# Kernel optimization log

Hardware: AMD Instinct MI355X
Metric: run time of the kernel (lower is better)

The kernel has to match this reference:

```python
import jax, jax.numpy as jnp
import numpy as np

D_MODEL = 1024
N_HEADS = 16
D_HEAD = D_MODEL // N_HEADS
BLOCK = 128
B, T = 2, 2048


def setup_inputs() -> dict:
    key = jax.random.key(0)
    ks = jax.random.split(key, 5)
    x = jax.random.normal(ks[0], (B, T, D_MODEL), dtype=jnp.float32)
    def init_w(k):
        # nn.Linear default init scale ~ 1/sqrt(fan_in)
        return jax.random.normal(k, (D_MODEL, D_MODEL), dtype=jnp.float32) / np.sqrt(D_MODEL).astype(np.float32)
    return {
        "x": x,
        "Wq": init_w(ks[1]),
        "Wk": init_w(ks[2]),
        "Wv": init_w(ks[3]),
        "Wo": init_w(ks[4]),
    }


def _flash_attention(Q, K, V, block_size, scale):
    """Online-softmax tiled attention over kv blocks (causal). Q,K,V: (B,H,T,d)."""
    Bb, H, Tt, d = Q.shape
    n_blocks = Tt // block_size
    # (n_blocks, B, H, block, d) so scan streams kv tiles
    Kb = K.reshape(Bb, H, n_blocks, block_size, d).transpose(2, 0, 1, 3, 4)
    Vb = V.reshape(Bb, H, n_blocks, block_size, d).transpose(2, 0, 1, 3, 4)
    starts = jnp.arange(n_blocks) * block_size
    q_pos = jnp.arange(Tt)

    def step(carry, xs):
        m, l, acc = carry
        kb, vb, st = xs
        # scores: (B,H,T,block)
        scores = scale * jnp.einsum('bhtd,bhsd->bhts', Q, kb)
        kv_pos = st + jnp.arange(block_size)
        future = kv_pos[None, :] > q_pos[:, None]          # (T, block)
        scores = jnp.where(future[None, None], -jnp.inf, scores)
        m_new = jnp.maximum(m, jnp.max(scores, axis=-1, keepdims=True))
        p = jnp.exp(scores - m_new)
        corr = jnp.exp(m - m_new)
        l = corr * l + jnp.sum(p, axis=-1, keepdims=True)
        acc = corr * acc + jnp.einsum('bhts,bhsd->bhtd', p, vb)
        return (m_new, l, acc), None

    m0 = jnp.full((Bb, H, Tt, 1), -jnp.inf, dtype=jnp.float32)
    l0 = jnp.zeros((Bb, H, Tt, 1), dtype=jnp.float32)
    a0 = jnp.zeros((Bb, H, Tt, d), dtype=jnp.float32)
    (m, l, acc), _ = jax.lax.scan(step, (m0, l0, a0), (Kb, Vb, starts))
    return acc / jnp.maximum(l, 1e-12)


def reference(x, Wq, Wk, Wv, Wo):
    Bx, Tx, _ = x.shape
    scale = 1.0 / np.sqrt(D_HEAD).astype(np.float32)
    def proj(W):  # nn.Linear: y = x @ W.T
        y = jnp.einsum('btm,nm->btn', x, W)
        return y.reshape(Bx, Tx, N_HEADS, D_HEAD).transpose(0, 2, 1, 3)
    Q, K, V = proj(Wq), proj(Wk), proj(Wv)
    O = _flash_attention(Q.astype(jnp.float32), K.astype(jnp.float32), V.astype(jnp.float32), BLOCK, scale)
    O = O.astype(x.dtype).transpose(0, 2, 1, 3).reshape(Bx, Tx, D_MODEL)
    return jnp.einsum('btm,nm->btn', O, Wo)
```

## Files before the change

### kernel.cpp

```cpp
#include <hip/hip_runtime.h>
#include <hip/hip_bf16.h>

typedef __attribute__((ext_vector_type(8))) short short8;
typedef __attribute__((ext_vector_type(4))) float f32x4;
typedef __attribute__((ext_vector_type(2))) unsigned int uint2v;
typedef __attribute__((ext_vector_type(4))) unsigned int uint4v;
typedef unsigned short u16;

#define MFMA_BF16(a, b, c) __builtin_amdgcn_mfma_f32_16x16x32_bf16(a, b, c, 0, 0, 0)

#define T_SEQ 2048
#define DMODEL 1024
#define NHEADS 16
#define DHEAD 64
#define NEG_BIG (-30000.0f)
#define QSCALE 0.1803368801111f
#define RESCALE_THR 8.0f

#if __has_builtin(__builtin_amdgcn_exp2f)
#define EXP2(x) __builtin_amdgcn_exp2f(x)
#else
#define EXP2(x) exp2f(x)
#endif

__device__ __forceinline__ unsigned bfr(unsigned u) {
  return (u + 0x7fffu + ((u >> 16) & 1u)) >> 16;
}
__device__ __forceinline__ uint4v ld8bf(const float* __restrict__ p) {
  const uint4v a = *(const uint4v*)p;
  const uint4v b = *(const uint4v*)(p + 4);
  uint4v r;
  r[0] = bfr(a[0]) | (bfr(a[1]) << 16);
  r[1] = bfr(a[2]) | (bfr(a[3]) << 16);
  r[2] = bfr(b[0]) | (bfr(b[1]) << 16);
  r[3] = bfr(b[2]) | (bfr(b[3]) << 16);
  return r;
}
__device__ __forceinline__ u16 f2bf(float f) {
  unsigned u = __float_as_uint(f);
  u += 0x7fffu + ((u >> 16) & 1u);
  return (u16)(u >> 16);
}
__device__ __forceinline__ void gld16(const u16* g, u16* l) {
  __builtin_amdgcn_global_load_lds(
      (const __attribute__((address_space(1))) unsigned int*)g,
      (__attribute__((address_space(3))) unsigned int*)l, 16, 0, 0);
}

__global__ __launch_bounds__(256) void cvt_all(
    const float* __restrict__ x, const float* __restrict__ wq,
    const float* __restrict__ wk, const float* __restrict__ wv,
    const float* __restrict__ wo, u16* __restrict__ xh, u16* __restrict__ wqh,
    u16* __restrict__ wkh, u16* __restrict__ wvh, u16* __restrict__ woh) {
  int bi = blockIdx.x;
  const float* s;
  u16* d;
  size_t base;
  if (bi < 2048) {
    s = x; d = xh; base = (size_t)bi * 2048;
  } else {
    int k = (bi - 2048) >> 9;
    int r = (bi - 2048) & 511;
    s = (k == 0) ? wq : (k == 1) ? wk : (k == 2) ? wv : wo;
    d = (k == 0) ? wqh : (k == 1) ? wkh : (k == 2) ? wvh : woh;
    base = (size_t)r * 2048;
  }
  size_t i = base + (size_t)threadIdx.x * 8;
  *(uint4v*)&d[i] = ld8bf(&s[i]);
}

__global__ __launch_bounds__(256) void gemm_qkv(
    const u16* __restrict__ X, const u16* __restrict__ Wq,
    const u16* __restrict__ Wk, const u16* __restrict__ Wv,
    u16* __restrict__ Qo, u16* __restrict__ Ko, u16* __restrict__ Vo) {
  __shared__ __attribute__((aligned(16))) u16 As[2][128 * 32];
  __shared__ __attribute__((aligned(16))) u16 Bs[2][128 * 32];
  const int tid = threadIdx.x, lane = tid & 63, w = tid >> 6;
  const int wm = (w >> 1) * 64, wn = (w & 1) * 64;
  const int lrow = lane & 15;
  const int lk = (lane >> 4) << 3;
  const int lq = (lane >> 4) << 2;
  const int mBase = blockIdx.x * 128, nBase = blockIdx.y * 128;
  const u16* Bt = (blockIdx.z == 0) ? Wq : (blockIdx.z == 1) ? Wk : Wv;
  u16* D = (blockIdx.z == 0) ? Qo : (blockIdx.z == 1) ? Ko : Vo;
  const float scale = (blockIdx.z == 0) ? QSCALE : 1.0f;

  f32x4 acc[4][4];
#pragma unroll
  for (int mi = 0; mi < 4; mi++)
#pragma unroll
    for (int ni = 0; ni < 4; ni++) acc[mi][ni] = (f32x4)0.0f;

  auto stage = [&](int buf, int k0) {
#pragma unroll
    for (int i = 0; i < 2; i++) {
      int c = i * 256 + tid;
      int r = c >> 2, kk = (c & 3) << 3;
      gld16(&X[(size_t)(mBase + r) * 1024 + k0 + kk], &As[buf][c * 8]);
      gld16(&Bt[(size_t)(nBase + r) * 1024 + k0 + kk], &Bs[buf][c * 8]);
    }
  };

  stage(0, 0);
  __syncthreads();
  int cur = 0;
  for (int k0 = 0; k0 < 1024; k0 += 32) {
    if (k0 + 32 < 1024) stage(cur ^ 1, k0 + 32);
    short8 af[4], bf[4];
#pragma unroll
    for (int mi = 0; mi < 4; mi++)
      af[mi] = *(const short8*)&As[cur][(wm + mi * 16 + lrow) * 32 + lk];
#pragma unroll
    for (int ni = 0; ni < 4; ni++)
      bf[ni] = *(const short8*)&Bs[cur][(wn + ni * 16 + lrow) * 32 + lk];
#pragma unroll
    for (int mi = 0; mi < 4; mi++)
#pragma unroll
      for (int ni = 0; ni < 4; ni++)
        acc[mi][ni] = MFMA_BF16(af[mi], bf[ni], acc[mi][ni]);
    __syncthreads();
    cur ^= 1;
  }
  const int vz = (blockIdx.z == 2);
#pragma unroll
  for (int mi = 0; mi < 4; mi++)
#pragma unroll
    for (int r = 0; r < 4; r++) {
      int m = mBase + wm + mi * 16 + lq + r;
      int b = m >> 11, t = m & 2047;
#pragma unroll
      for (int ni = 0; ni < 4; ni++) {
        int n = nBase + wn + ni * 16 + lrow;
        int h = n >> 6, dd = n & 63;
        size_t idx = vz ? (((size_t)((b * NHEADS + h) * DHEAD + dd)) * T_SEQ + t)
                        : ((((size_t)(b * NHEADS + h)) * T_SEQ + t) * DHEAD + dd);
        D[idx] = f2bf(acc[mi][ni][r] * scale);
      }
    }
}

__global__ __launch_bounds__(256) void attn_snake(
    const u16* __restrict__ Qg, const u16* __restrict__ Kg,
    const u16* __restrict__ Vtg, u16* __restrict__ Ob) {
  __shared__ __attribute__((aligned(16))) u16 smem[20992];
  u16* Qs = smem;
  u16* Ps = smem;

  const int tid = threadIdx.x;
  const int w = tid >> 6, lane = tid & 63;
  const int lrow = lane & 15;
  const int quad = lane >> 4;
  const int lk = quad << 3;
  const int rsw = lrow & 7;
  const int q_local = w * 16 + lrow;

  const int j = blockIdx.x;
  const int bh = blockIdx.y;
  const int b = bh >> 4, h = bh & 15;
  const u16* Qp = Qg + (size_t)bh * T_SEQ * DHEAD;
  const u16* Kp = Kg + (size_t)bh * T_SEQ * DHEAD;
  const u16* Vp = Vtg + (size_t)bh * DHEAD * T_SEQ;

  auto stage_kv = [&](u16* Ksd, u16* Vtd, int kvb) {
#pragma unroll
    for (int i = 0; i < 2; i++) {
      int c = i * 256 + tid;
      int r = c >> 3;
      int sw = ((c & 7) ^ (r & 7)) << 3;
      gld16(&Kp[(size_t)(kvb + r) * DHEAD + sw], &Ksd[c * 8]);
      gld16(&Vp[(size_t)r * T_SEQ + kvb + sw], &Vtd[c * 8]);
    }
  };

#pragma unroll
  for (int p = 0; p < 2; p++) {
    const int qt = p ? (31 - j) : j;
    const int qb = qt * 64;

    __syncthreads();
#pragma unroll
    for (int i = 0; i < 2; i++) {
      int c = i * 256 + tid;
      int r = c >> 3, kk = (c & 7) << 3;
      *(uint4v*)&Qs[r * 72 + kk] =
          *(const uint4v*)&Qp[(size_t)(qb + r) * DHEAD + kk];
    }
    stage_kv(smem + 4608, smem + 12800, 0);
    __syncthreads();

    short8 qf[2];
#pragma unroll
    for (int ks = 0; ks < 2; ks++)
      qf[ks] = *(const short8*)&Qs[q_local * 72 + ks * 32 + lk];

    float mst = NEG_BIG, lst = 0.f;
    f32x4 oacc[4];
#pragma unroll
    for (int nd = 0; nd < 4; nd++) oacc[nd] = (f32x4)0.0f;

    const int ntiles = qt + 1;
    int cur = 0;
    for (int kt = 0; kt < ntiles; kt++) {
      u16* Ksc = smem + 4608 + cur * 4096;
      u16* Vtc = smem + 12800 + cur * 4096;
      if (kt + 1 < ntiles)
        stage_kv(smem + 4608 + (cur ^ 1) * 4096,
                 smem + 12800 + (cur ^ 1) * 4096, (kt + 1) * 64);

      f32x4 s[4];
      __builtin_amdgcn_s_setprio(1);
#pragma unroll
      for (int kvt = 0; kvt < 4; kvt++) {
        f32x4 a = (f32x4)0.0f;
#pragma unroll
        for (int ks = 0; ks < 2; ks++) {
          short8 kf = *(const short8*)&Ksc[(kvt * 16 + lrow) * 64 +
                                           ((((ks << 2) + quad) ^ rsw) << 3)];
          a = MFMA_BF16(kf, qf[ks], a);
        }
        s[kvt] = a;
      }
      __builtin_amdgcn_s_setprio(0);

      if (kt == qt) {
#pragma unroll
        for (int kvt = 0; kvt < 4; kvt++)
#pragma unroll
          for (int r = 0; r < 4; r++)
            if (kvt * 16 + quad * 4 + r > q_local) s[kvt][r] = NEG_BIG;
      }

      float mx = s[0][0];
#pragma unroll
      for (int kvt = 0; kvt < 4; kvt++)
#pragma unroll
        for (int r = 0; r < 4; r++) mx = fmaxf(mx, s[kvt][r]);
      mx = fmaxf(mx, __shfl_xor(mx, 16));
      mx = fmaxf(mx, __shfl_xor(mx, 32));
      if (!__all(mx <= mst + RESCALE_THR)) {
        float mn = fmaxf(mst, mx);
        float corr = EXP2(mst - mn);
        mst = mn;
        lst *= corr;
#pragma unroll
        for (int nd = 0; nd < 4; nd++) oacc[nd] *= corr;
      }
      float ls = 0.f;
#pragma unroll
      for (int kvt = 0; kvt < 4; kvt++)
#pragma unroll
        for (int r = 0; r < 4; r++) {
          float pv = EXP2(s[kvt][r] - mst);
          s[kvt][r] = pv;
          ls += pv;
        }
      ls += __shfl_xor(ls, 16);
      ls += __shfl_xor(ls, 32);
      lst += ls;

#pragma unroll
      for (int kvt = 0; kvt < 4; kvt++) {
        uint2v pk;
        pk[0] = (__float_as_uint(s[kvt][0]) >> 16) |
                (__float_as_uint(s[kvt][1]) & 0xffff0000u);
        pk[1] = (__float_as_uint(s[kvt][2]) >> 16) |
                (__float_as_uint(s[kvt][3]) & 0xffff0000u);
        *(uint2v*)&Ps[q_local * 72 + kvt * 16 + quad * 4] = pk;
      }

      __builtin_amdgcn_s_setprio(1);
#pragma unroll
      for (int ks = 0; ks < 2; ks++) {
        short8 pf = *(const short8*)&Ps[q_local * 72 + ks * 32 + lk];
#pragma unroll
        for (int nd = 0; nd < 4; nd++) {
          short8 vf = *(const short8*)&Vtc[(nd * 16 + lrow) * 64 +
                                           ((((ks << 2) + quad) ^ rsw) << 3)];
          oacc[nd] = MFMA_BF16(vf, pf, oacc[nd]);
        }
      }
      __builtin_amdgcn_s_setprio(0);

      __syncthreads();
      cur ^= 1;
    }

    float inv = 1.f / lst;
    size_t rowbase = ((size_t)(b * T_SEQ + qb + q_local)) * DMODEL + h * DHEAD;
#pragma unroll
    for (int nd = 0; nd < 4; nd++) {
      uint2v pk;
      pk[0] = (unsigned)f2bf(oacc[nd][0] * inv) |
              ((unsigned)f2bf(oacc[nd][1] * inv) << 16);
      pk[1] = (unsigned)f2bf(oacc[nd][2] * inv) |
              ((unsigned)f2bf(oacc[nd][3] * inv) << 16);
      *(uint2v*)&Ob[rowbase + nd * 16 + quad * 4] = pk;
    }
  }
}

__global__ __launch_bounds__(256) void gemm_out_bf(const u16* __restrict__ O,
                                                   const u16* __restrict__ Wo,
                                                   float* __restrict__ Out) {
  __shared__ __attribute__((aligned(16))) u16 As[2][128 * 32];
  __shared__ __attribute__((aligned(16))) u16 Bs[2][128 * 32];
  const int tid = threadIdx.x, lane = tid & 63, w = tid >> 6;
  const int wm = (w >> 1) * 64, wn = (w & 1) * 64;
  const int lrow = lane & 15;
  const int lk = (lane >> 4) << 3;
  const int lq = (lane >> 4) << 2;
  const int mBase = blockIdx.x * 128, nBase = blockIdx.y * 128;

  f32x4 acc[4][4];
#pragma unroll
  for (int mi = 0; mi < 4; mi++)
#pragma unroll
    for (int ni = 0; ni < 4; ni++) acc[mi][ni] = (f32x4)0.0f;

  auto stage = [&](int buf, int k0) {
#pragma unroll
    for (int i = 0; i < 2; i++) {
      int c = i * 256 + tid;
      int r = c >> 2, kk = (c & 3) << 3;
      gld16(&O[(size_t)(mBase + r) * 1024 + k0 + kk], &As[buf][c * 8]);
      gld16(&Wo[(size_t)(nBase + r) * 1024 + k0 + kk], &Bs[buf][c * 8]);
    }
  };

  stage(0, 0);
  __syncthreads();
  int cur = 0;
  for (int k0 = 0; k0 < 1024; k0 += 32) {
    if (k0 + 32 < 1024) stage(cur ^ 1, k0 + 32);
    short8 af[4], bf[4];
#pragma unroll
    for (int mi = 0; mi < 4; mi++)
      af[mi] = *(const short8*)&As[cur][(wm + mi * 16 + lrow) * 32 + lk];
#pragma unroll
    for (int ni = 0; ni < 4; ni++)
      bf[ni] = *(const short8*)&Bs[cur][(wn + ni * 16 + lrow) * 32 + lk];
#pragma unroll
    for (int mi = 0; mi < 4; mi++)
#pragma unroll
      for (int ni = 0; ni < 4; ni++)
        acc[mi][ni] = MFMA_BF16(af[mi], bf[ni], acc[mi][ni]);
    __syncthreads();
    cur ^= 1;
  }
#pragma unroll
  for (int mi = 0; mi < 4; mi++)
#pragma unroll
    for (int r = 0; r < 4; r++) {
      int m = mBase + wm + mi * 16 + lq + r;
#pragma unroll
      for (int ni = 0; ni < 4; ni++)
        Out[(size_t)m * DMODEL + nBase + wn + ni * 16 + lrow] = acc[mi][ni][r];
    }
}

extern "C" void kernel_launch(void* const* d_in, const int* in_sizes, int n_in,
                              void* d_out, int out_size, void* d_ws,
                              size_t ws_size, hipStream_t stream) {
  const float* x = (const float*)d_in[0];
  const float* Wq = (const float*)d_in[1];
  const float* Wk = (const float*)d_in[2];
  const float* Wv = (const float*)d_in[3];
  const float* Wo = (const float*)d_in[4];
  float* out = (float*)d_out;

  u16* xh = (u16*)d_ws;
  u16* wqh = xh + 4194304;
  u16* wkh = wqh + 1048576;
  u16* wvh = wkh + 1048576;
  u16* woh = wvh + 1048576;
  u16* Q = woh + 1048576;
  u16* K = Q + 4194304;
  u16* V = K + 4194304;
  u16* O = V + 4194304;

  cvt_all<<<dim3(4096), 256, 0, stream>>>(x, Wq, Wk, Wv, Wo, xh, wqh, wkh, wvh, woh);
  gemm_qkv<<<dim3(32, 8, 3), 256, 0, stream>>>(xh, wqh, wkh, wvh, Q, K, V);
  attn_snake<<<dim3(16, 32), 256, 0, stream>>>(Q, K, V, O);
  gemm_out_bf<<<dim3(32, 8), 256, 0, stream>>>(O, woh, out);
}
```

Before: 186.8 us.

## Load attention K/V fragments straight to registers and shrink output GEMM tile

The attention kernel no longer stages Q, K and V tiles through shared memory with a block-wide barrier each iteration. Each wave now loads its MFMA fragments directly from global memory into registers, prefetching the next tile after the current MFMAs. Shared memory is kept only for P, and the grid is flattened with a remapped block index so nearby blocks share a head. The output GEMM uses 128x64 tiles to launch twice as many blocks. In exchange, every wave reads K and V separately from global or L2 memory instead of sharing one staged copy, and more registers are in use.

Measured after the change: 265.9 us. 42.4% more time.

```diff
diff --git a/kernel.cpp b/kernel.cpp
--- a/kernel.cpp
+++ b/kernel.cpp
@@ -139,59 +139,50 @@
     }
 }
 
-__global__ __launch_bounds__(256) void attn_snake(
+__global__ __launch_bounds__(256, 2) void attn_snake(
     const u16* __restrict__ Qg, const u16* __restrict__ Kg,
     const u16* __restrict__ Vtg, u16* __restrict__ Ob) {
-  __shared__ __attribute__((aligned(16))) u16 smem[20992];
-  u16* Qs = smem;
-  u16* Ps = smem;
+  __shared__ __attribute__((aligned(16))) u16 Ps[64 * 72];
 
   const int tid = threadIdx.x;
   const int w = tid >> 6, lane = tid & 63;
   const int lrow = lane & 15;
   const int quad = lane >> 4;
   const int lk = quad << 3;
-  const int rsw = lrow & 7;
   const int q_local = w * 16 + lrow;
 
-  const int j = blockIdx.x;
-  const int bh = blockIdx.y;
+  const int id = blockIdx.x;
+  const int j = (id >> 3) & 15;
+  const int bh = (id & 7) * 4 + ((id >> 7) & 3);
   const int b = bh >> 4, h = bh & 15;
   const u16* Qp = Qg + (size_t)bh * T_SEQ * DHEAD;
   const u16* Kp = Kg + (size_t)bh * T_SEQ * DHEAD;
   const u16* Vp = Vtg + (size_t)bh * DHEAD * T_SEQ;
 
-  auto stage_kv = [&](u16* Ksd, u16* Vtd, int kvb) {
-#pragma unroll
-    for (int i = 0; i < 2; i++) {
-      int c = i * 256 + tid;
-      int r = c >> 3;
-      int sw = ((c & 7) ^ (r & 7)) << 3;
-      gld16(&Kp[(size_t)(kvb + r) * DHEAD + sw], &Ksd[c * 8]);
-      gld16(&Vp[(size_t)r * T_SEQ + kvb + sw], &Vtd[c * 8]);
-    }
-  };
+  const unsigned kof = (unsigned)lrow * 64 + quad * 8;
+  const unsigned vof = (unsigned)lrow * 2048 + quad * 8;
 
 #pragma unroll
   for (int p = 0; p < 2; p++) {
     const int qt = p ? (31 - j) : j;
     const int qb = qt * 64;
 
-    __syncthreads();
-#pragma unroll
-    for (int i = 0; i < 2; i++) {
-      int c = i * 256 + tid;
-      int r = c >> 3, kk = (c & 7) << 3;
-      *(uint4v*)&Qs[r * 72 + kk] =
-          *(const uint4v*)&Qp[(size_t)(qb + r) * DHEAD + kk];
-    }
-    stage_kv(smem + 4608, smem + 12800, 0);
-    __syncthreads();
-
     short8 qf[2];
 #pragma unroll
     for (int ks = 0; ks < 2; ks++)
-      qf[ks] = *(const short8*)&Qs[q_local * 72 + ks * 32 + lk];
+      qf[ks] = *(const short8*)&Qp[(unsigned)(qb + q_local) * 64 + ks * 32 + lk];
+
+    short8 kf[4][2], vf[2][4];
+#pragma unroll
+    for (int kvt = 0; kvt < 4; kvt++)
+#pragma unroll
+      for (int ks = 0; ks < 2; ks++)
+        kf[kvt][ks] = *(const short8*)&Kp[kof + kvt * 1024 + ks * 32];
+#pragma unroll
+    for (int ks = 0; ks < 2; ks++)
+#pragma unroll
+      for (int nd = 0; nd < 4; nd++)
+        vf[ks][nd] = *(const short8*)&Vp[vof + nd * 32768 + ks * 32];
 
     float mst = NEG_BIG, lst = 0.f;
     f32x4 oacc[4];
@@ -199,28 +190,26 @@
     for (int nd = 0; nd < 4; nd++) oacc[nd] = (f32x4)0.0f;
 
     const int ntiles = qt + 1;
-    int cur = 0;
     for (int kt = 0; kt < ntiles; kt++) {
-      u16* Ksc = smem + 4608 + cur * 4096;
-      u16* Vtc = smem + 12800 + cur * 4096;
-      if (kt + 1 < ntiles)
-        stage_kv(smem + 4608 + (cur ^ 1) * 4096,
-                 smem + 12800 + (cur ^ 1) * 4096, (kt + 1) * 64);
-
       f32x4 s[4];
       __builtin_amdgcn_s_setprio(1);
 #pragma unroll
       for (int kvt = 0; kvt < 4; kvt++) {
         f32x4 a = (f32x4)0.0f;
 #pragma unroll
-        for (int ks = 0; ks < 2; ks++) {
-          short8 kf = *(const short8*)&Ksc[(kvt * 16 + lrow) * 64 +
-                                           ((((ks << 2) + quad) ^ rsw) << 3)];
-          a = MFMA_BF16(kf, qf[ks], a);
-        }
+        for (int ks = 0; ks < 2; ks++) a = MFMA_BF16(kf[kvt][ks], qf[ks], a);
         s[kvt] = a;
       }
       __builtin_amdgcn_s_setprio(0);
+
+      if (kt + 1 < ntiles) {
+        const unsigned kn = kof + (unsigned)(kt + 1) * 4096;
+#pragma unroll
+        for (int kvt = 0; kvt < 4; kvt++)
+#pragma unroll
+          for (int ks = 0; ks < 2; ks++)
+            kf[kvt][ks] = *(const short8*)&Kp[kn + kvt * 1024 + ks * 32];
+      }
 
       if (kt == qt) {
 #pragma unroll
@@ -273,16 +262,19 @@
       for (int ks = 0; ks < 2; ks++) {
         short8 pf = *(const short8*)&Ps[q_local * 72 + ks * 32 + lk];
 #pragma unroll
-        for (int nd = 0; nd < 4; nd++) {
-          short8 vf = *(const short8*)&Vtc[(nd * 16 + lrow) * 64 +
-                                           ((((ks << 2) + quad) ^ rsw) << 3)];
-          oacc[nd] = MFMA_BF16(vf, pf, oacc[nd]);
-        }
+        for (int nd = 0; nd < 4; nd++)
+          oacc[nd] = MFMA_BF16(vf[ks][nd], pf, oacc[nd]);
       }
       __builtin_amdgcn_s_setprio(0);
 
-      __syncthreads();
-      cur ^= 1;
+      if (kt + 1 < ntiles) {
+        const unsigned vn = vof + (unsigned)(kt + 1) * 64;
+#pragma unroll
+        for (int ks = 0; ks < 2; ks++)
+#pragma unroll
+          for (int nd = 0; nd < 4; nd++)
+            vf[ks][nd] = *(const short8*)&Vp[vn + nd * 32768 + ks * 32];
+      }
     }
 
     float inv = 1.f / lst;
@@ -303,19 +295,19 @@
                                                    const u16* __restrict__ Wo,
                                                    float* __restrict__ Out) {
   __shared__ __attribute__((aligned(16))) u16 As[2][128 * 32];
-  __shared__ __attribute__((aligned(16))) u16 Bs[2][128 * 32];
+  __shared__ __attribute__((aligned(16))) u16 Bs[2][64 * 32];
   const int tid = threadIdx.x, lane = tid & 63, w = tid >> 6;
-  const int wm = (w >> 1) * 64, wn = (w & 1) * 64;
+  const int wm = (w >> 1) * 64, wn = (w & 1) * 32;
   const int lrow = lane & 15;
   const int lk = (lane >> 4) << 3;
   const int lq = (lane >> 4) << 2;
-  const int mBase = blockIdx.x * 128, nBase = blockIdx.y * 128;
-
-  f32x4 acc[4][4];
+  const int mBase = blockIdx.x * 128, nBase = blockIdx.y * 64;
+
+  f32x4 acc[4][2];
 #pragma unroll
   for (int mi = 0; mi < 4; mi++)
 #pragma unroll
-    for (int ni = 0; ni < 4; ni++) acc[mi][ni] = (f32x4)0.0f;
+    for (int ni = 0; ni < 2; ni++) acc[mi][ni] = (f32x4)0.0f;
 
   auto stage = [&](int buf, int k0) {
 #pragma unroll
@@ -323,8 +315,9 @@
       int c = i * 256 + tid;
       int r = c >> 2, kk = (c & 3) << 3;
       gld16(&O[(size_t)(mBase + r) * 1024 + k0 + kk], &As[buf][c * 8]);
-      gld16(&Wo[(size_t)(nBase + r) * 1024 + k0 + kk], &Bs[buf][c * 8]);
-    }
+    }
+    int r = tid >> 2, kk = (tid & 3) << 3;
+    gld16(&Wo[(size_t)(nBase + r) * 1024 + k0 + kk], &Bs[buf][tid * 8]);
   };
 
   stage(0, 0);
@@ -332,17 +325,17 @@
   int cur = 0;
   for (int k0 = 0; k0 < 1024; k0 += 32) {
     if (k0 + 32 < 1024) stage(cur ^ 1, k0 + 32);
-    short8 af[4], bf[4];
+    short8 af[4], bf[2];
 #pragma unroll
     for (int mi = 0; mi < 4; mi++)
       af[mi] = *(const short8*)&As[cur][(wm + mi * 16 + lrow) * 32 + lk];
 #pragma unroll
-    for (int ni = 0; ni < 4; ni++)
+    for (int ni = 0; ni < 2; ni++)
       bf[ni] = *(const short8*)&Bs[cur][(wn + ni * 16 + lrow) * 32 + lk];
 #pragma unroll
     for (int mi = 0; mi < 4; mi++)
 #pragma unroll
-      for (int ni = 0; ni < 4; ni++)
+      for (int ni = 0; ni < 2; ni++)
         acc[mi][ni] = MFMA_BF16(af[mi], bf[ni], acc[mi][ni]);
     __syncthreads();
     cur ^= 1;
@@ -353,7 +346,7 @@
     for (int r = 0; r < 4; r++) {
       int m = mBase + wm + mi * 16 + lq + r;
 #pragma unroll
-      for (int ni = 0; ni < 4; ni++)
+      for (int ni = 0; ni < 2; ni++)
         Out[(size_t)m * DMODEL + nBase + wn + ni * 16 + lrow] = acc[mi][ni][r];
     }
 }
@@ -380,6 +373,6 @@
 
   cvt_all<<<dim3(4096), 256, 0, stream>>>(x, Wq, Wk, Wv, Wo, xh, wqh, wkh, wvh, woh);
   gemm_qkv<<<dim3(32, 8, 3), 256, 0, stream>>>(xh, wqh, wkh, wvh, Q, K, V);
-  attn_snake<<<dim3(16, 32), 256, 0, stream>>>(Q, K, V, O);
-  gemm_out_bf<<<dim3(32, 8), 256, 0, stream>>>(O, woh, out);
-}
+  attn_snake<<<dim3(512), 256, 0, stream>>>(Q, K, V, O);
+  gemm_out_bf<<<dim3(32, 16), 256, 0, stream>>>(O, woh, out);
+}
```
